# Optimization experiments

Hardware: AMD Instinct MI355X
Metric: run time of the kernel (lower is better)

## Reference

```python
import jax, jax.numpy as jnp
import numpy as np

PENALTY_FACTOR = 2.0
THRESHOLD = 0.01


def setup_inputs() -> dict:
    key = jax.random.key(0)
    k1, k2 = jax.random.split(key)
    B, N = 256, 65536
    prediction = jax.random.normal(k1, (B, N), dtype=jnp.float32)
    label = jax.random.normal(k2, (B, N), dtype=jnp.float32)
    return {"prediction": prediction, "label": label}


def _first_last_significant(mask, half):
    # mask: [B, half] bool. Returns per-row first/last True index,
    # defaulting to (0, half-1) when the row has no True entries
    # (matching the torch fallback branch).
    any_m = jnp.any(mask, axis=1)
    first = jnp.argmax(mask, axis=1)                      # 0 if all False
    last = (half - 1) - jnp.argmax(mask[:, ::-1], axis=1)  # half-1 if all False
    first = jnp.where(any_m, first, 0)
    last = jnp.where(any_m, last, half - 1)
    return first, last


def reference(prediction, label):
    B, N = label.shape
    half = N // 2
    label_real, label_imag = label[:, :half], label[:, half:]
    pred_real, pred_imag = prediction[:, :half], prediction[:, half:]

    label_phase = jnp.arctan2(label_imag, label_real)
    pred_phase = jnp.arctan2(pred_imag, pred_real)
    label_int = label_real ** 2 + label_imag ** 2
    pred_int = pred_real ** 2 + pred_imag ** 2

    fr, lr = _first_last_significant(jnp.abs(label_real) > THRESHOLD, half)
    fi, li = _first_last_significant(jnp.abs(label_imag) > THRESHOLD, half)

    idx = jnp.arange(half)[None, :]  # [1, half]
    w_real = jnp.where((idx < fr[:, None]) | (idx > lr[:, None]), PENALTY_FACTOR, 1.0)
    w_imag = jnp.where((idx < fi[:, None]) | (idx > li[:, None]), PENALTY_FACTOR, 1.0)

    mse_real = w_real * (pred_real - label_real) ** 2
    mse_imag = w_imag * (pred_imag - label_imag) ** 2
    mse_int = (pred_int - label_int) ** 2
    mse_phase = (pred_phase - label_phase) ** 2

    per_sample = (mse_real.mean(axis=1) + mse_imag.mean(axis=1)
                  + 50.0 * mse_int.mean(axis=1) + 0.0 * mse_phase.mean(axis=1))
    return per_sample.mean()
```

## Files before the change

### kernel.cpp

```cpp
#include <hip/hip_runtime.h>
#include <climits>

constexpr int HALF = 32768;
constexpr int TPB  = 256;
constexpr int SEG  = 4096;
constexpr int NSEG = HALF / SEG;
constexpr int NPASS = SEG / 4 / TPB;
constexpr float THRESH = 0.01f;

__global__ __launch_bounds__(TPB)
void main_kernel(const float* __restrict__ pred, const float* __restrict__ label,
                 float* __restrict__ part_sum, int4* __restrict__ part_idx)
{
    const int seg = blockIdx.x, row = blockIdx.y;
    const int t = threadIdx.x, wave = t >> 6, lane = t & 63;

    const size_t rb4 = (size_t)row * (size_t)(2 * HALF / 4);
    const int sb4 = seg * (SEG / 4);
    const float4* lr4 = (const float4*)label + rb4 + sb4;
    const float4* li4 = lr4 + (HALF / 4);
    const float4* pr4 = (const float4*)pred + rb4 + sb4;
    const float4* pi4 = pr4 + (HALF / 4);

    float sum = 0.f;
    int minr = INT_MAX, maxr = -1, mini = INT_MAX, maxi = -1;

    #pragma unroll
    for (int p = 0; p < NPASS; ++p) {
        const int v = p * TPB + t;
        float4 a = lr4[v], b = li4[v], pp = pr4[v], q = pi4[v];
        const int base = seg * SEG + v * 4;

#define STEP(ax, bx, px, qx, idx)                              \
        {                                                      \
            float dr = (px) - (ax), di = (qx) - (bx);          \
            float lint = (ax) * (ax) + (bx) * (bx);            \
            float pint = (px) * (px) + (qx) * (qx);            \
            float dd = pint - lint;                            \
            sum += dr * dr + di * di + 50.f * dd * dd;         \
            if (fabsf(ax) > THRESH) {                          \
                minr = min(minr, (idx)); maxr = max(maxr, (idx)); \
            }                                                  \
            if (fabsf(bx) > THRESH) {                          \
                mini = min(mini, (idx)); maxi = max(maxi, (idx)); \
            }                                                  \
        }
        STEP(a.x, b.x, pp.x, q.x, base + 0)
        STEP(a.y, b.y, pp.y, q.y, base + 1)
        STEP(a.z, b.z, pp.z, q.z, base + 2)
        STEP(a.w, b.w, pp.w, q.w, base + 3)
#undef STEP
    }

    #pragma unroll
    for (int off = 32; off > 0; off >>= 1) {
        sum  += __shfl_down(sum, off);
        minr  = min(minr, __shfl_down(minr, off));
        maxr  = max(maxr, __shfl_down(maxr, off));
        mini  = min(mini, __shfl_down(mini, off));
        maxi  = max(maxi, __shfl_down(maxi, off));
    }

    __shared__ float s_sum[4];
    __shared__ int s_idx[4][4];
    if (lane == 0) {
        s_sum[wave] = sum;
        s_idx[wave][0] = minr; s_idx[wave][1] = maxr;
        s_idx[wave][2] = mini; s_idx[wave][3] = maxi;
    }
    __syncthreads();
    if (t == 0) {
        float S = 0.f; int mr = INT_MAX, Mr = -1, mi = INT_MAX, Mi = -1;
        #pragma unroll
        for (int w = 0; w < 4; ++w) {
            S += s_sum[w];
            mr = min(mr, s_idx[w][0]); Mr = max(Mr, s_idx[w][1]);
            mi = min(mi, s_idx[w][2]); Mi = max(Mi, s_idx[w][3]);
        }
        const int slot = row * NSEG + seg;
        part_sum[slot] = S;
        part_idx[slot] = make_int4(mr, Mr, mi, Mi);
    }
}

__global__ __launch_bounds__(TPB)
void edge_kernel(const float* __restrict__ pred, const float* __restrict__ label,
                 const float* __restrict__ part_sum, const int4* __restrict__ part_idx,
                 float* __restrict__ row_tot)
{
    const int row = blockIdx.x;
    const int t = threadIdx.x, wave = t >> 6, lane = t & 63;

    float base = 0.f;
    int fr = INT_MAX, lastr = -1, fi = INT_MAX, lasti = -1;
    #pragma unroll
    for (int s = 0; s < NSEG; ++s) {
        base += part_sum[row * NSEG + s];
        int4 v = part_idx[row * NSEG + s];
        fr = min(fr, v.x); lastr = max(lastr, v.y);
        fi = min(fi, v.z); lasti = max(lasti, v.w);
    }
    if (lastr < 0) { fr = 0; lastr = HALF - 1; }
    if (lasti < 0) { fi = 0; lasti = HALF - 1; }

    const float* Lr = label + (size_t)row * (2 * HALF);
    const float* Li = Lr + HALF;
    const float* Pr = pred + (size_t)row * (2 * HALF);
    const float* Pi = Pr + HALF;

    float ex = 0.f;
    for (int i = t; i < fr; i += TPB)             { float d = Pr[i] - Lr[i]; ex += d * d; }
    for (int i = lastr + 1 + t; i < HALF; i += TPB) { float d = Pr[i] - Lr[i]; ex += d * d; }
    for (int i = t; i < fi; i += TPB)             { float d = Pi[i] - Li[i]; ex += d * d; }
    for (int i = lasti + 1 + t; i < HALF; i += TPB) { float d = Pi[i] - Li[i]; ex += d * d; }

    #pragma unroll
    for (int off = 32; off > 0; off >>= 1) ex += __shfl_down(ex, off);
    __shared__ float s_ex[4];
    if (lane == 0) s_ex[wave] = ex;
    __syncthreads();
    if (t == 0)
        row_tot[row] = base + s_ex[0] + s_ex[1] + s_ex[2] + s_ex[3];
}

__global__ void finalize_kernel(const float* __restrict__ row_tot,
                                float* __restrict__ out, int rows)
{
    const int t = threadIdx.x;
    float v = 0.f;
    for (int i = t; i < rows; i += 256) v += row_tot[i];
    #pragma unroll
    for (int off = 32; off > 0; off >>= 1) v += __shfl_down(v, off);
    __shared__ float s[4];
    if ((t & 63) == 0) s[t >> 6] = v;
    __syncthreads();
    if (t == 0)
        out[0] = (s[0] + s[1] + s[2] + s[3]) * (1.0f / ((float)HALF * (float)rows));
}

extern "C" void kernel_launch(void* const* d_in, const int* in_sizes, int n_in,
                              void* d_out, int out_size, void* d_ws, size_t ws_size,
                              hipStream_t stream) {
    const float* pred  = (const float*)d_in[0];
    const float* label = (const float*)d_in[1];
    float* out = (float*)d_out;

    const int rows = in_sizes[0] / (2 * HALF);
    const int nslots = rows * NSEG;

    float* part_sum = (float*)d_ws;
    int4*  part_idx = (int4*)((char*)d_ws + nslots * 4);
    float* row_tot  = (float*)((char*)d_ws + nslots * 4 + nslots * 16);

    dim3 gridA(NSEG, rows);
    main_kernel<<<gridA, TPB, 0, stream>>>(pred, label, part_sum, part_idx);
    edge_kernel<<<rows, TPB, 0, stream>>>(pred, label, part_sum, part_idx, row_tot);
    finalize_kernel<<<1, 256, 0, stream>>>(row_tot, out, rows);
}
```

Baseline: 28.69 us.

## Merge edge and finalize kernels into one tail block and shrink main segments

The main kernel now processes a single float4 per thread per block, giving more blocks per row, and stores partials segment-major. The per-row edge kernel and the finalize kernel are combined into one single-block tail kernel where each thread serially scans its row's penalty edges and the block reduces to the final output. This removes a kernel launch and an intermediate buffer, but the tail kernel assumes rows <= 256 and does serial per-thread scans, which would be slow if edge regions were long.

```diff
diff --git a/kernel.cpp b/kernel.cpp
--- a/kernel.cpp
+++ b/kernel.cpp
@@ -3,9 +3,7 @@
 
 constexpr int HALF = 32768;
 constexpr int TPB  = 256;
-constexpr int SEG  = 4096;
-constexpr int NSEG = HALF / SEG;
-constexpr int NPASS = SEG / 4 / TPB;
+constexpr int NSEG = HALF / 4 / TPB;
 constexpr float THRESH = 0.01f;
 
 __global__ __launch_bounds__(TPB)
@@ -16,53 +14,50 @@
     const int t = threadIdx.x, wave = t >> 6, lane = t & 63;
 
     const size_t rb4 = (size_t)row * (size_t)(2 * HALF / 4);
-    const int sb4 = seg * (SEG / 4);
-    const float4* lr4 = (const float4*)label + rb4 + sb4;
-    const float4* li4 = lr4 + (HALF / 4);
-    const float4* pr4 = (const float4*)pred + rb4 + sb4;
-    const float4* pi4 = pr4 + (HALF / 4);
+    const int v = seg * TPB + t;
+    const float4* lr4 = (const float4*)label + rb4;
+    const float4* pr4 = (const float4*)pred + rb4;
 
+    float4 a  = lr4[v];
+    float4 b  = lr4[v + HALF / 4];
+    float4 pp = pr4[v];
+    float4 q  = pr4[v + HALF / 4];
+
+    const int base = v * 4;
     float sum = 0.f;
     int minr = INT_MAX, maxr = -1, mini = INT_MAX, maxi = -1;
 
-    #pragma unroll
-    for (int p = 0; p < NPASS; ++p) {
-        const int v = p * TPB + t;
-        float4 a = lr4[v], b = li4[v], pp = pr4[v], q = pi4[v];
-        const int base = seg * SEG + v * 4;
-
-#define STEP(ax, bx, px, qx, idx)                              \
-        {                                                      \
-            float dr = (px) - (ax), di = (qx) - (bx);          \
-            float lint = (ax) * (ax) + (bx) * (bx);            \
-            float pint = (px) * (px) + (qx) * (qx);            \
-            float dd = pint - lint;                            \
-            sum += dr * dr + di * di + 50.f * dd * dd;         \
-            if (fabsf(ax) > THRESH) {                          \
-                minr = min(minr, (idx)); maxr = max(maxr, (idx)); \
-            }                                                  \
-            if (fabsf(bx) > THRESH) {                          \
-                mini = min(mini, (idx)); maxi = max(maxi, (idx)); \
-            }                                                  \
-        }
-        STEP(a.x, b.x, pp.x, q.x, base + 0)
-        STEP(a.y, b.y, pp.y, q.y, base + 1)
-        STEP(a.z, b.z, pp.z, q.z, base + 2)
-        STEP(a.w, b.w, pp.w, q.w, base + 3)
+#define STEP(ax, bx, px, qx, idx)                                 \
+    {                                                             \
+        float dr = (px) - (ax), di = (qx) - (bx);                 \
+        float lint = (ax) * (ax) + (bx) * (bx);                   \
+        float pint = (px) * (px) + (qx) * (qx);                   \
+        float dd = pint - lint;                                   \
+        sum += dr * dr + di * di + 50.f * dd * dd;                \
+        if (fabsf(ax) > THRESH) {                                 \
+            minr = min(minr, (idx)); maxr = max(maxr, (idx));     \
+        }                                                         \
+        if (fabsf(bx) > THRESH) {                                 \
+            mini = min(mini, (idx)); maxi = max(maxi, (idx));     \
+        }                                                         \
+    }
+    STEP(a.x, b.x, pp.x, q.x, base + 0)
+    STEP(a.y, b.y, pp.y, q.y, base + 1)
+    STEP(a.z, b.z, pp.z, q.z, base + 2)
+    STEP(a.w, b.w, pp.w, q.w, base + 3)
 #undef STEP
-    }
 
     #pragma unroll
     for (int off = 32; off > 0; off >>= 1) {
-        sum  += __shfl_down(sum, off);
-        minr  = min(minr, __shfl_down(minr, off));
-        maxr  = max(maxr, __shfl_down(maxr, off));
-        mini  = min(mini, __shfl_down(mini, off));
-        maxi  = max(maxi, __shfl_down(maxi, off));
+        sum += __shfl_down(sum, off);
+        minr = min(minr, __shfl_down(minr, off));
+        maxr = max(maxr, __shfl_down(maxr, off));
+        mini = min(mini, __shfl_down(mini, off));
+        maxi = max(maxi, __shfl_down(maxi, off));
     }
 
     __shared__ float s_sum[4];
-    __shared__ int s_idx[4][4];
+    __shared__ int   s_idx[4][4];
     if (lane == 0) {
         s_sum[wave] = sum;
         s_idx[wave][0] = minr; s_idx[wave][1] = maxr;
@@ -77,62 +72,50 @@
             mr = min(mr, s_idx[w][0]); Mr = max(Mr, s_idx[w][1]);
             mi = min(mi, s_idx[w][2]); Mi = max(Mi, s_idx[w][3]);
         }
-        const int slot = row * NSEG + seg;
+        const int slot = seg * gridDim.y + row;
         part_sum[slot] = S;
         part_idx[slot] = make_int4(mr, Mr, mi, Mi);
     }
 }
 
 __global__ __launch_bounds__(TPB)
-void edge_kernel(const float* __restrict__ pred, const float* __restrict__ label,
+void tail_kernel(const float* __restrict__ pred, const float* __restrict__ label,
                  const float* __restrict__ part_sum, const int4* __restrict__ part_idx,
-                 float* __restrict__ row_tot)
+                 float* __restrict__ out, int rows)
 {
-    const int row = blockIdx.x;
     const int t = threadIdx.x, wave = t >> 6, lane = t & 63;
 
-    float base = 0.f;
-    int fr = INT_MAX, lastr = -1, fi = INT_MAX, lasti = -1;
-    #pragma unroll
-    for (int s = 0; s < NSEG; ++s) {
-        base += part_sum[row * NSEG + s];
-        int4 v = part_idx[row * NSEG + s];
-        fr = min(fr, v.x); lastr = max(lastr, v.y);
-        fi = min(fi, v.z); lasti = max(lasti, v.w);
+    float total = 0.f;
+    if (t < rows) {
+        float S = 0.f;
+        int fr = INT_MAX, lastr = -1, fi = INT_MAX, lasti = -1;
+        for (int s = 0; s < NSEG; ++s) {
+            const int slot = s * rows + t;
+            S += part_sum[slot];
+            int4 v = part_idx[slot];
+            fr = min(fr, v.x); lastr = max(lastr, v.y);
+            fi = min(fi, v.z); lasti = max(lasti, v.w);
+        }
+        if (lastr < 0) { fr = 0; lastr = HALF - 1; }
+        if (lasti < 0) { fi = 0; lasti = HALF - 1; }
+
+        const float* Lr = label + (size_t)t * (2 * HALF);
+        const float* Li = Lr + HALF;
+        const float* Pr = pred + (size_t)t * (2 * HALF);
+        const float* Pi = Pr + HALF;
+
+        for (int i = 0; i < fr; ++i)            { float d = Pr[i] - Lr[i]; S += d * d; }
+        for (int i = lastr + 1; i < HALF; ++i)  { float d = Pr[i] - Lr[i]; S += d * d; }
+        for (int i = 0; i < fi; ++i)            { float d = Pi[i] - Li[i]; S += d * d; }
+        for (int i = lasti + 1; i < HALF; ++i)  { float d = Pi[i] - Li[i]; S += d * d; }
+
+        total = S;
     }
-    if (lastr < 0) { fr = 0; lastr = HALF - 1; }
-    if (lasti < 0) { fi = 0; lasti = HALF - 1; }
-
-    const float* Lr = label + (size_t)row * (2 * HALF);
-    const float* Li = Lr + HALF;
-    const float* Pr = pred + (size_t)row * (2 * HALF);
-    const float* Pi = Pr + HALF;
-
-    float ex = 0.f;
-    for (int i = t; i < fr; i += TPB)             { float d = Pr[i] - Lr[i]; ex += d * d; }
-    for (int i = lastr + 1 + t; i < HALF; i += TPB) { float d = Pr[i] - Lr[i]; ex += d * d; }
-    for (int i = t; i < fi; i += TPB)             { float d = Pi[i] - Li[i]; ex += d * d; }
-    for (int i = lasti + 1 + t; i < HALF; i += TPB) { float d = Pi[i] - Li[i]; ex += d * d; }
 
     #pragma unroll
-    for (int off = 32; off > 0; off >>= 1) ex += __shfl_down(ex, off);
-    __shared__ float s_ex[4];
-    if (lane == 0) s_ex[wave] = ex;
-    __syncthreads();
-    if (t == 0)
-        row_tot[row] = base + s_ex[0] + s_ex[1] + s_ex[2] + s_ex[3];
-}
-
-__global__ void finalize_kernel(const float* __restrict__ row_tot,
-                                float* __restrict__ out, int rows)
-{
-    const int t = threadIdx.x;
-    float v = 0.f;
-    for (int i = t; i < rows; i += 256) v += row_tot[i];
-    #pragma unroll
-    for (int off = 32; off > 0; off >>= 1) v += __shfl_down(v, off);
+    for (int off = 32; off > 0; off >>= 1) total += __shfl_down(total, off);
     __shared__ float s[4];
-    if ((t & 63) == 0) s[t >> 6] = v;
+    if (lane == 0) s[wave] = total;
     __syncthreads();
     if (t == 0)
         out[0] = (s[0] + s[1] + s[2] + s[3]) * (1.0f / ((float)HALF * (float)rows));
@@ -150,10 +133,8 @@
 
     float* part_sum = (float*)d_ws;
     int4*  part_idx = (int4*)((char*)d_ws + nslots * 4);
-    float* row_tot  = (float*)((char*)d_ws + nslots * 4 + nslots * 16);
 
     dim3 gridA(NSEG, rows);
     main_kernel<<<gridA, TPB, 0, stream>>>(pred, label, part_sum, part_idx);
-    edge_kernel<<<rows, TPB, 0, stream>>>(pred, label, part_sum, part_idx, row_tot);
-    finalize_kernel<<<1, 256, 0, stream>>>(row_tot, out, rows);
+    tail_kernel<<<1, TPB, 0, stream>>>(pred, label, part_sum, part_idx, out, rows);
 }
```

New measurement: 29.48 us. +2.8%, slower.
